# Kernel tuning notes

Hardware: AMD Instinct MI355X
Metric: run time of the kernel (lower is better)

Reference implementation:

```python
import jax, jax.numpy as jnp
import numpy as np

CROSSOVER_MAGNITUDE = 0.3
MUTATION_FACTOR = 0.3

B, A, H = 16, 512, 8  # batch, activation_size (== dim_emb), n_head


def setup_inputs() -> dict:
    key = jax.random.key(0)
    ks = jax.random.split(key, 11)
    d = A
    s = 0.02  # small init scale for weights
    return {
        "Q": jax.random.normal(ks[0], (B, A, A), jnp.float32),
        "K": jax.random.normal(ks[1], (B, A, A), jnp.float32),
        "V": jax.random.normal(ks[2], (B, A), jnp.float32),
        "WQ_w": jax.random.normal(ks[3], (d, d), jnp.float32) * s,
        "WQ_b": jax.random.normal(ks[4], (d,), jnp.float32) * s,
        "WK_w": jax.random.normal(ks[5], (d, d), jnp.float32) * s,
        "WK_b": jax.random.normal(ks[6], (d,), jnp.float32) * s,
        "WV_w": jax.random.normal(ks[7], (d, d), jnp.float32) * s,
        "WV_b": jax.random.normal(ks[8], (d,), jnp.float32) * s,
        "WO_w": jax.random.normal(ks[9], (d, d * H), jnp.float32) * s,
        "WO_b": jax.random.normal(ks[10], (d,), jnp.float32) * s,
    }


def _attention_core(Qp, Kp, Vp, WO_w, WO_b):
    # Qp, Kp: (B, A, A) projected; identical across heads in the original
    # (heads are copies stacked before shared Linear), so compute once
    # and broadcast. Vp: (B, A).
    rkey = jax.random.key(42)
    kp, km, kr1, kr2 = jax.random.split(rkey, 4)

    am0 = jnp.einsum('bji,bjk->bik', Qp, Kp) / jnp.sqrt(jnp.float32(8.0))
    am = jnp.broadcast_to(am0[:, None], (B, H, A, A))  # (B,H,A,A)

    def mutate(a):
        # elementwise multiply by U(1-mf, 1+mf) noise
        m = jax.random.uniform(km, a.shape, jnp.float32,
                               1.0 - MUTATION_FACTOR, 1.0 + MUTATION_FACTOR)
        return a * m

    def crossover(a):
        # swap the tail segments [c:] of two random rows per (batch, head)
        c = A - int(A * CROSSOVER_MAGNITUDE)
        r1 = jax.random.randint(kr1, (B, H), 0, A)
        r2 = jax.random.randint(kr2, (B, H), 0, A)
        bi = jnp.arange(B)[:, None]
        hi = jnp.arange(H)[None, :]
        tails = a[..., c:]                     # (B,H,A,A-c)
        t1 = tails[bi, hi, r1]                 # (B,H,A-c)
        t2 = tails[bi, hi, r2]
        tails = tails.at[bi, hi, r1].set(t2).at[bi, hi, r2].set(t1)
        return jnp.concatenate([a[..., :c], tails], axis=-1)

    p = jax.random.uniform(kp, ())
    am = jax.lax.cond(p <= 0.6, mutate, crossover, am)

    attn = jax.nn.softmax(am, axis=-1)               # (B,H,A,A)
    out = jnp.einsum('bhij,bj->bhi', attn, Vp)       # attn @ V[...,None] squeezed
    out = out.reshape(B, H * A)
    return out @ WO_w.T + WO_b                       # (B, A)


def reference(Q, K, V, WQ_w, WQ_b, WK_w, WK_b, WV_w, WV_b, WO_w, WO_b):
    Qp = Q @ WQ_w.T + WQ_b   # (B,A,A), same for every head
    Kp = K @ WK_w.T + WK_b
    Vp = V @ WV_w.T + WV_b   # (B,A)
    return _attention_core(Qp, Kp, Vp, WO_w, WO_b)
```

## Files before the change

### kernel.cpp

```cpp
#include <hip/hip_runtime.h>
#include <stdint.h>
#include <string.h>

#define B_ 16
#define A_ 512
#define H_ 8
#define C_CROSS 359
#define LDSTRIDE 40

typedef short short8 __attribute__((ext_vector_type(8)));
typedef float floatx4 __attribute__((ext_vector_type(4)));

__host__ __device__ __forceinline__ uint32_t rotl32(uint32_t x, int r) {
#ifdef __HIP_DEVICE_COMPILE__
  return __builtin_amdgcn_alignbit(x, x, 32 - r);
#else
  return (x << r) | (x >> (32 - r));
#endif
}

__host__ __device__ __forceinline__ void tf2x32(uint32_t k0, uint32_t k1,
                                                uint32_t x0, uint32_t x1,
                                                uint32_t& o0, uint32_t& o1) {
  uint32_t ks2 = k0 ^ k1 ^ 0x1BD11BDAu;
  x0 += k0; x1 += k1;
#define TFR(r) { x0 += x1; x1 = rotl32(x1, r); x1 ^= x0; }
  TFR(13) TFR(15) TFR(26) TFR(6)   x0 += k1;  x1 += ks2 + 1u;
  TFR(17) TFR(29) TFR(16) TFR(24)  x0 += ks2; x1 += k0 + 2u;
  TFR(13) TFR(15) TFR(26) TFR(6)   x0 += k0;  x1 += k1 + 3u;
  TFR(17) TFR(29) TFR(16) TFR(24)  x0 += k1;  x1 += ks2 + 4u;
  TFR(13) TFR(15) TFR(26) TFR(6)   x0 += ks2; x1 += k0 + 5u;
#undef TFR
  o0 = x0; o1 = x1;
}

__host__ __device__ __forceinline__ float bits2u01(uint32_t bits) {
  uint32_t v = (bits >> 9) | 0x3f800000u;
  float f;
#ifdef __HIP_DEVICE_COMPILE__
  f = __uint_as_float(v);
#else
  memcpy(&f, &v, 4);
#endif
  return f - 1.0f;
}

__device__ __forceinline__ float mutval(uint32_t km0, uint32_t km1, uint32_t L) {
  uint32_t a, b;
  tf2x32(km0, km1, 0u, L, a, b);
  float u = bits2u01(a ^ b);
  return fmaxf(0.7f, u * (1.3f - 0.7f) + 0.7f);
}

__device__ __forceinline__ uint32_t f2bf(float x) {
  uint32_t u = __float_as_uint(x);
  return (u + 0x7fffu + ((u >> 16) & 1u)) >> 16;
}
__device__ __forceinline__ float bf2f(uint32_t h) {
  return __uint_as_float(h << 16);
}

__device__ __forceinline__ void split8(const float* p, short8& h, short8& l) {
  float4 v0 = *(const float4*)p;
  float4 v1 = *(const float4*)(p + 4);
  float xs[8] = {v0.x, v0.y, v0.z, v0.w, v1.x, v1.y, v1.z, v1.w};
#pragma unroll
  for (int j = 0; j < 8; ++j) {
    uint32_t hb = f2bf(xs[j]);
    h[j] = (short)hb;
    l[j] = (short)f2bf(xs[j] - bf2f(hb));
  }
}

__global__ __launch_bounds__(256, 2) void lin_mfma2(
    const float* __restrict__ Xq, const float* __restrict__ Wq,
    const float* __restrict__ bq, ushort* __restrict__ QptH, ushort* __restrict__ QptL,
    const float* __restrict__ Xk, const float* __restrict__ Wk,
    const float* __restrict__ bk, ushort* __restrict__ KptH, ushort* __restrict__ KptL) {
  int bid = blockIdx.x;
  int z = bid >> 8;
  int rem = bid & 255;
  int ti = rem >> 2, tn = rem & 3;
  const float* X = z ? Xk : Xq;
  const float* W = z ? Wk : Wq;
  const float* bias = z ? bk : bq;
  ushort* OH = z ? KptH : QptH;
  ushort* OL = z ? KptL : QptL;

  __shared__ __align__(16) char smem[40960];
  ushort (*Ah)[LDSTRIDE] = (ushort(*)[LDSTRIDE])(smem);
  ushort (*Al)[LDSTRIDE] = (ushort(*)[LDSTRIDE])(smem + 10240);
  ushort (*Bh)[LDSTRIDE] = (ushort(*)[LDSTRIDE])(smem + 20480);
  ushort (*Bl)[LDSTRIDE] = (ushort(*)[LDSTRIDE])(smem + 30720);
  uint32_t (*cs)[132] = (uint32_t(*)[132])(smem);

  int tid = threadIdx.x;
  int w = tid >> 6, lane = tid & 63, quad = lane >> 4, l16 = lane & 15;
  int wm = (w >> 1) * 64, wn = (w & 1) * 64;
  int m0 = ti * 128;
  int n0 = tn * 128;

  float bv[4];
#pragma unroll
  for (int nt = 0; nt < 4; ++nt) bv[nt] = bias[n0 + wn + nt * 16 + l16];

  floatx4 acc[4][4] = {};

  for (int k0 = 0; k0 < 512; k0 += 32) {
    short8 ha[2], la[2], hb[2], lb[2];
#pragma unroll
    for (int g = 0; g < 2; ++g) {
      int gid = g * 256 + tid;
      int m = gid >> 2, kg = gid & 3;
      split8(X + (size_t)(m0 + m) * 512 + k0 + kg * 8, ha[g], la[g]);
      split8(W + (size_t)(n0 + m) * 512 + k0 + kg * 8, hb[g], lb[g]);
    }
    __syncthreads();
#pragma unroll
    for (int g = 0; g < 2; ++g) {
      int gid = g * 256 + tid;
      int m = gid >> 2, kg = gid & 3;
      *(short8*)&Ah[m][kg * 8] = ha[g];
      *(short8*)&Al[m][kg * 8] = la[g];
      *(short8*)&Bh[m][kg * 8] = hb[g];
      *(short8*)&Bl[m][kg * 8] = lb[g];
    }
    __syncthreads();
    short8 fAh[4], fAl[4], fBh[4], fBl[4];
#pragma unroll
    for (int t4 = 0; t4 < 4; ++t4) {
      int ma = wm + t4 * 16 + l16;
      int nb = wn + t4 * 16 + l16;
      fAh[t4] = *(const short8*)&Ah[ma][quad * 8];
      fAl[t4] = *(const short8*)&Al[ma][quad * 8];
      fBh[t4] = *(const short8*)&Bh[nb][quad * 8];
      fBl[t4] = *(const short8*)&Bl[nb][quad * 8];
    }
#pragma unroll
    for (int mt = 0; mt < 4; ++mt)
#pragma unroll
      for (int nt = 0; nt < 4; ++nt) {
        acc[mt][nt] = __builtin_amdgcn_mfma_f32_16x16x32_bf16(fAh[mt], fBh[nt], acc[mt][nt], 0, 0, 0);
        acc[mt][nt] = __builtin_amdgcn_mfma_f32_16x16x32_bf16(fAh[mt], fBl[nt], acc[mt][nt], 0, 0, 0);
        acc[mt][nt] = __builtin_amdgcn_mfma_f32_16x16x32_bf16(fAl[mt], fBh[nt], acc[mt][nt], 0, 0, 0);
      }
  }

  __syncthreads();
  int bb = m0 >> 9, i0 = m0 & 511;
  for (int p = 0; p < 2; ++p) {
    if ((w & 1) == p) {
#pragma unroll
      for (int mt = 0; mt < 4; ++mt)
#pragma unroll
        for (int nt = 0; nt < 4; ++nt)
#pragma unroll
          for (int rr = 0; rr < 4; ++rr) {
            float val = acc[mt][nt][rr] + bv[nt];
            uint32_t hb2 = f2bf(val);
            uint32_t lb2 = f2bf(val - bf2f(hb2));
            cs[nt * 16 + l16][wm + mt * 16 + quad * 4 + rr] = (hb2 << 16) | lb2;
          }
    }
    __syncthreads();
    {
      int col_l = tid >> 2, iseg = (tid & 3) * 32;
      int d = n0 + p * 64 + col_l;
      size_t obase = ((size_t)(bb * 512 + d)) * 512 + i0 + iseg;
      ushort* oh = OH + obase;
      ushort* ol = OL + obase;
#pragma unroll
      for (int sgi = 0; sgi < 4; ++sgi) {
        short8 hv, lv;
#pragma unroll
        for (int j = 0; j < 8; ++j) {
          uint32_t v = cs[col_l][iseg + sgi * 8 + j];
          hv[j] = (short)(v >> 16);
          lv[j] = (short)(v & 0xffffu);
        }
        *(short8*)(oh + sgi * 8) = hv;
        *(short8*)(ol + sgi * 8) = lv;
      }
    }
    __syncthreads();
  }
}

__global__ __launch_bounds__(256) void am_mfma2(
    const ushort* __restrict__ QH, const ushort* __restrict__ QL,
    const ushort* __restrict__ KH, const ushort* __restrict__ KL,
    float* __restrict__ am0) {
  int bid = blockIdx.x;
  int xcd = bid & 7, slot = bid >> 3;
  int bz = xcd + 8 * (slot >> 4);
  int tt = slot & 15, ti = tt >> 2, tk = tt & 3;
  int bm0 = ti * 128, bn0 = tk * 128;
  size_t base = (size_t)bz * 262144;
  const ushort* AHp = QH + base + (size_t)bm0 * 512;
  const ushort* ALp = QL + base + (size_t)bm0 * 512;
  const ushort* BHp = KH + base + (size_t)bn0 * 512;
  const ushort* BLp = KL + base + (size_t)bn0 * 512;

  __shared__ __align__(16) char smem[40960];
  ushort (*Ah)[LDSTRIDE] = (ushort(*)[LDSTRIDE])(smem);
  ushort (*Al)[LDSTRIDE] = (ushort(*)[LDSTRIDE])(smem + 10240);
  ushort (*Bh)[LDSTRIDE] = (ushort(*)[LDSTRIDE])(smem + 20480);
  ushort (*Bl)[LDSTRIDE] = (ushort(*)[LDSTRIDE])(smem + 30720);

  int tid = threadIdx.x;
  int w = tid >> 6, lane = tid & 63, quad = lane >> 4, l16 = lane & 15;
  int wm = (w >> 1) * 64, wn = (w & 1) * 64;

  floatx4 acc[4][4] = {};

  for (int k0 = 0; k0 < 512; k0 += 32) {
    short8 ha[2], la[2], hb[2], lb[2];
#pragma unroll
    for (int g = 0; g < 2; ++g) {
      int gid = g * 256 + tid;
      int m = gid >> 2, kg = gid & 3;
      size_t off = (size_t)m * 512 + k0 + kg * 8;
      ha[g] = *(const short8*)(AHp + off);
      la[g] = *(const short8*)(ALp + off);
      hb[g] = *(const short8*)(BHp + off);
      lb[g] = *(const short8*)(BLp + off);
    }
    __syncthreads();
#pragma unroll
    for (int g = 0; g < 2; ++g) {
      int gid = g * 256 + tid;
      int m = gid >> 2, kg = gid & 3;
      *(short8*)&Ah[m][kg * 8] = ha[g];
      *(short8*)&Al[m][kg * 8] = la[g];
      *(short8*)&Bh[m][kg * 8] = hb[g];
      *(short8*)&Bl[m][kg * 8] = lb[g];
    }
    __syncthreads();
    short8 fAh[4], fAl[4], fBh[4], fBl[4];
#pragma unroll
    for (int t4 = 0; t4 < 4; ++t4) {
      int ma = wm + t4 * 16 + l16;
      int nb = wn + t4 * 16 + l16;
      fAh[t4] = *(const short8*)&Ah[ma][quad * 8];
      fAl[t4] = *(const short8*)&Al[ma][quad * 8];
      fBh[t4] = *(const short8*)&Bh[nb][quad * 8];
      fBl[t4] = *(const short8*)&Bl[nb][quad * 8];
    }
#pragma unroll
    for (int mt = 0; mt < 4; ++mt)
#pragma unroll
      for (int nt = 0; nt < 4; ++nt) {
        acc[mt][nt] = __builtin_amdgcn_mfma_f32_16x16x32_bf16(fAh[mt], fBh[nt], acc[mt][nt], 0, 0, 0);
        acc[mt][nt] = __builtin_amdgcn_mfma_f32_16x16x32_bf16(fAh[mt], fBl[nt], acc[mt][nt], 0, 0, 0);
        acc[mt][nt] = __builtin_amdgcn_mfma_f32_16x16x32_bf16(fAl[mt], fBh[nt], acc[mt][nt], 0, 0, 0);
      }
  }
  const float scale = 0.35355339059327373f;
#pragma unroll
  for (int mt = 0; mt < 4; ++mt)
#pragma unroll
    for (int nt = 0; nt < 4; ++nt)
#pragma unroll
      for (int rr = 0; rr < 4; ++rr) {
        int row = bm0 + wm + mt * 16 + quad * 4 + rr;
        int col = bn0 + wn + nt * 16 + l16;
        am0[((size_t)(bz * 512 + row)) * 512 + col] = acc[mt][nt][rr] * scale;
      }
}

__global__ __launch_bounds__(256) void small_gemm(
    const float* __restrict__ X, const float* __restrict__ W,
    const float* __restrict__ bias, float* __restrict__ out, int K) {
  __shared__ float xs[16 * 260];
  __shared__ float ws[16 * 260];
  int tid = threadIdx.x;
  int j0 = blockIdx.x * 16;
  int k0 = blockIdx.y * 256;
#pragma unroll
  for (int it = 0; it < 4; ++it) {
    int idx = it * 256 + tid;
    int rr = idx >> 6, kk4 = idx & 63;
    float4 xv = *(const float4*)(X + (size_t)rr * K + k0 + kk4 * 4);
    float4 wv = *(const float4*)(W + (size_t)(j0 + rr) * K + k0 + kk4 * 4);
    *(float4*)&xs[rr * 260 + kk4 * 4] = xv;
    *(float4*)&ws[rr * 260 + kk4 * 4] = wv;
  }
  __syncthreads();
  int b = tid & 15, j = tid >> 4;
  const float* xr = &xs[b * 260];
  const float* wr = &ws[j * 260];
  float acc = 0.f;
#pragma unroll
  for (int kk = 0; kk < 256; kk += 4) {
    float4 a = *(const float4*)(xr + kk);
    float4 w4 = *(const float4*)(wr + kk);
    acc += a.x * w4.x + a.y * w4.y + a.z * w4.z + a.w * w4.w;
  }
  if (blockIdx.y == 0) acc += bias[j0 + j];
  atomicAdd(&out[b * 512 + j0 + j], acc);
}

__global__ __launch_bounds__(256) void soft_mut(
    const float* __restrict__ am0, const float* __restrict__ Vp,
    float* __restrict__ oa, uint32_t km0, uint32_t km1) {
  int tid = threadIdx.x;
  int w = tid >> 6, lane = tid & 63;
  int rrow = blockIdx.x * 4 + w;
  int b = rrow >> 12, h = (rrow >> 9) & 7, i = rrow & 511;
  const float* ar = am0 + ((size_t)((b << 9) + i)) * A_;
  const float* vr = Vp + (b << 9);
  uint32_t Lb = ((uint32_t)(((b * 8 + h) << 9) + i)) << 9;
  float x[8], vv[8];
#pragma unroll
  for (int j = 0; j < 8; ++j) {
    int k = lane + 64 * j;
    float a = ar[k];
    vv[j] = vr[k];
    x[j] = a * mutval(km0, km1, Lb + (uint32_t)k);
  }
  float s = 0.f, wsum = 0.f;
#pragma unroll
  for (int j = 0; j < 8; ++j) {
    float e = __expf(x[j]);
    s += e;
    wsum += e * vv[j];
  }
#pragma unroll
  for (int o = 32; o; o >>= 1) { s += __shfl_xor(s, o); wsum += __shfl_xor(wsum, o); }
  if (lane == 0) oa[(((size_t)(b * 8 + h)) << 9) + i] = wsum / s;
}

struct CrossCfg { int r1[B_ * H_]; int r2[B_ * H_]; };

__global__ __launch_bounds__(256) void soft_cross(
    const float* __restrict__ am0, const float* __restrict__ Vp,
    float* __restrict__ oa, CrossCfg cfg) {
  int tid = threadIdx.x;
  int w = tid >> 6, lane = tid & 63;
  int rrow = blockIdx.x * 4 + w;
  int b = rrow >> 12, h = (rrow >> 9) & 7, i = rrow & 511;
  int rr1 = cfg.r1[b * 8 + h], rr2 = cfg.r2[b * 8 + h];
  int src = (i == rr2) ? rr1 : ((i == rr1) ? rr2 : i);
  const float* ar = am0 + ((size_t)((b << 9) + i)) * A_;
  const float* ar2 = am0 + ((size_t)((b << 9) + src)) * A_;
  const float* vr = Vp + (b << 9);
  float x[8], vv[8];
#pragma unroll
  for (int j = 0; j < 8; ++j) {
    int k = lane + 64 * j;
    vv[j] = vr[k];
    x[j] = (k >= C_CROSS) ? ar2[k] : ar[k];
  }
  float s = 0.f, wsum = 0.f;
#pragma unroll
  for (int j = 0; j < 8; ++j) {
    float e = __expf(x[j]);
    s += e;
    wsum += e * vv[j];
  }
#pragma unroll
  for (int o = 32; o; o >>= 1) { s += __shfl_xor(s, o); wsum += __shfl_xor(wsum, o); }
  if (lane == 0) oa[(((size_t)(b * 8 + h)) << 9) + i] = wsum / s;
}

extern "C" void kernel_launch(void* const* d_in, const int* in_sizes, int n_in,
                              void* d_out, int out_size, void* d_ws, size_t ws_size,
                              hipStream_t stream) {
  (void)in_sizes; (void)n_in; (void)out_size; (void)ws_size;
  const float* Q    = (const float*)d_in[0];
  const float* K    = (const float*)d_in[1];
  const float* V    = (const float*)d_in[2];
  const float* WQ_w = (const float*)d_in[3];
  const float* WQ_b = (const float*)d_in[4];
  const float* WK_w = (const float*)d_in[5];
  const float* WK_b = (const float*)d_in[6];
  const float* WV_w = (const float*)d_in[7];
  const float* WV_b = (const float*)d_in[8];
  const float* WO_w = (const float*)d_in[9];
  const float* WO_b = (const float*)d_in[10];
  float* out = (float*)d_out;

  char* ws = (char*)d_ws;
  ushort* QptH = (ushort*)(ws);
  ushort* QptL = (ushort*)(ws + (size_t)8388608);
  ushort* KptH = (ushort*)(ws + (size_t)16777216);
  ushort* KptL = (ushort*)(ws + (size_t)25165824);
  float*  am0  = (float*) (ws + (size_t)33554432);
  float*  Vp   = (float*) (ws + (size_t)50331648);
  float*  oa   = (float*) (ws + (size_t)50331648 + 65536);

  uint32_t kp0, kp1, km0, km1, kr10, kr11, kr20, kr21, a, bbits;
  tf2x32(0u, 42u, 0u, 0u, kp0, kp1);
  tf2x32(0u, 42u, 0u, 1u, km0, km1);
  tf2x32(0u, 42u, 0u, 2u, kr10, kr11);
  tf2x32(0u, 42u, 0u, 3u, kr20, kr21);
  tf2x32(kp0, kp1, 0u, 0u, a, bbits);
  float p = bits2u01(a ^ bbits);
  if (p < 0.f) p = 0.f;
  bool mutate = (p <= 0.6f);

  hipMemsetAsync(Vp, 0, 16 * 512 * sizeof(float), stream);
  hipMemsetAsync(out, 0, 16 * 512 * sizeof(float), stream);

  lin_mfma2<<<512, 256, 0, stream>>>(Q, WQ_w, WQ_b, QptH, QptL,
                                     K, WK_w, WK_b, KptH, KptL);
  small_gemm<<<dim3(32, 2), 256, 0, stream>>>(V, WV_w, WV_b, Vp, 512);
  am_mfma2<<<256, 256, 0, stream>>>(QptH, QptL, KptH, KptL, am0);
  if (mutate) {
    soft_mut<<<16384, 256, 0, stream>>>(am0, Vp, oa, km0, km1);
  } else {
    CrossCfg cfg;
    uint32_t c0, c1;
    tf2x32(kr10, kr11, 0u, 1u, c0, c1);
    for (int t = 0; t < B_ * H_; ++t) {
      tf2x32(c0, c1, 0u, (uint32_t)t, a, bbits);
      cfg.r1[t] = (int)((a ^ bbits) & 511u);
    }
    tf2x32(kr20, kr21, 0u, 1u, c0, c1);
    for (int t = 0; t < B_ * H_; ++t) {
      tf2x32(c0, c1, 0u, (uint32_t)t, a, bbits);
      cfg.r2[t] = (int)((a ^ bbits) & 511u);
    }
    soft_cross<<<16384, 256, 0, stream>>>(am0, Vp, oa, cfg);
  }
  small_gemm<<<dim3(32, 16), 256, 0, stream>>>(oa, WO_w, WO_b, out, 4096);
}
```

Before: 250.7 us.

## Prefetch next K-tile into registers in GEMM kernels and simplify bf16 splitting

Both MFMA GEMM kernels now load the next K-slice from global memory into registers right after the LDS write barrier, so those loads overlap the MFMA work of the current slice. The fp32-to-bf16 hi/lo split switches from round-to-nearest to truncation, which needs fewer integer operations. am_mfma2 gets a min-blocks-per-CU launch bound of 2. The softmax kernels fuse the RNG and exp into a single loop with a folded FMA. Prefetching raises register pressure. Truncating the hi part slightly changes the hi/lo precision split.

```diff
diff --git a/kernel.cpp b/kernel.cpp
--- a/kernel.cpp
+++ b/kernel.cpp
@@ -45,30 +45,21 @@
   return f - 1.0f;
 }
 
-__device__ __forceinline__ float mutval(uint32_t km0, uint32_t km1, uint32_t L) {
-  uint32_t a, b;
-  tf2x32(km0, km1, 0u, L, a, b);
-  float u = bits2u01(a ^ b);
-  return fmaxf(0.7f, u * (1.3f - 0.7f) + 0.7f);
-}
-
-__device__ __forceinline__ uint32_t f2bf(float x) {
+__device__ __forceinline__ void tsplit(float x, short& h, short& l) {
   uint32_t u = __float_as_uint(x);
-  return (u + 0x7fffu + ((u >> 16) & 1u)) >> 16;
-}
-__device__ __forceinline__ float bf2f(uint32_t h) {
-  return __uint_as_float(h << 16);
-}
-
-__device__ __forceinline__ void split8(const float* p, short8& h, short8& l) {
-  float4 v0 = *(const float4*)p;
-  float4 v1 = *(const float4*)(p + 4);
+  float hf = __uint_as_float(u & 0xffff0000u);
+  h = (short)(u >> 16);
+  l = (short)(__float_as_uint(x - hf) >> 16);
+}
+
+__device__ __forceinline__ void tsplit8(const float4& v0, const float4& v1,
+                                        short8& h, short8& l) {
   float xs[8] = {v0.x, v0.y, v0.z, v0.w, v1.x, v1.y, v1.z, v1.w};
 #pragma unroll
   for (int j = 0; j < 8; ++j) {
-    uint32_t hb = f2bf(xs[j]);
-    h[j] = (short)hb;
-    l[j] = (short)f2bf(xs[j] - bf2f(hb));
+    short hh, ll;
+    tsplit(xs[j], hh, ll);
+    h[j] = hh; l[j] = ll;
   }
 }
 
@@ -104,28 +95,52 @@
 #pragma unroll
   for (int nt = 0; nt < 4; ++nt) bv[nt] = bias[n0 + wn + nt * 16 + l16];
 
+  const float* pX[2];
+  const float* pW[2];
+  int mW[2], kgW[2];
+#pragma unroll
+  for (int g = 0; g < 2; ++g) {
+    int gid = g * 256 + tid;
+    int m = gid >> 2, kg = gid & 3;
+    mW[g] = m; kgW[g] = kg;
+    pX[g] = X + (size_t)(m0 + m) * 512 + kg * 8;
+    pW[g] = W + (size_t)(n0 + m) * 512 + kg * 8;
+  }
+
+  float4 ra[2][2], rb[2][2];
+#pragma unroll
+  for (int g = 0; g < 2; ++g) {
+    ra[g][0] = *(const float4*)(pX[g]);
+    ra[g][1] = *(const float4*)(pX[g] + 4);
+    rb[g][0] = *(const float4*)(pW[g]);
+    rb[g][1] = *(const float4*)(pW[g] + 4);
+  }
+
   floatx4 acc[4][4] = {};
 
   for (int k0 = 0; k0 < 512; k0 += 32) {
-    short8 ha[2], la[2], hb[2], lb[2];
+    __syncthreads();
 #pragma unroll
     for (int g = 0; g < 2; ++g) {
-      int gid = g * 256 + tid;
-      int m = gid >> 2, kg = gid & 3;
-      split8(X + (size_t)(m0 + m) * 512 + k0 + kg * 8, ha[g], la[g]);
-      split8(W + (size_t)(n0 + m) * 512 + k0 + kg * 8, hb[g], lb[g]);
-    }
-    __syncthreads();
-#pragma unroll
-    for (int g = 0; g < 2; ++g) {
-      int gid = g * 256 + tid;
-      int m = gid >> 2, kg = gid & 3;
-      *(short8*)&Ah[m][kg * 8] = ha[g];
-      *(short8*)&Al[m][kg * 8] = la[g];
-      *(short8*)&Bh[m][kg * 8] = hb[g];
-      *(short8*)&Bl[m][kg * 8] = lb[g];
-    }
-    __syncthreads();
+      short8 h8, l8;
+      tsplit8(ra[g][0], ra[g][1], h8, l8);
+      *(short8*)&Ah[mW[g]][kgW[g] * 8] = h8;
+      *(short8*)&Al[mW[g]][kgW[g] * 8] = l8;
+      tsplit8(rb[g][0], rb[g][1], h8, l8);
+      *(short8*)&Bh[mW[g]][kgW[g] * 8] = h8;
+      *(short8*)&Bl[mW[g]][kgW[g] * 8] = l8;
+    }
+    __syncthreads();
+    if (k0 < 480) {
+      int kn = k0 + 32;
+#pragma unroll
+      for (int g = 0; g < 2; ++g) {
+        ra[g][0] = *(const float4*)(pX[g] + kn);
+        ra[g][1] = *(const float4*)(pX[g] + kn + 4);
+        rb[g][0] = *(const float4*)(pW[g] + kn);
+        rb[g][1] = *(const float4*)(pW[g] + kn + 4);
+      }
+    }
     short8 fAh[4], fAl[4], fBh[4], fBl[4];
 #pragma unroll
     for (int t4 = 0; t4 < 4; ++t4) {
@@ -157,9 +172,10 @@
 #pragma unroll
           for (int rr = 0; rr < 4; ++rr) {
             float val = acc[mt][nt][rr] + bv[nt];
-            uint32_t hb2 = f2bf(val);
-            uint32_t lb2 = f2bf(val - bf2f(hb2));
-            cs[nt * 16 + l16][wm + mt * 16 + quad * 4 + rr] = (hb2 << 16) | lb2;
+            uint32_t u = __float_as_uint(val);
+            uint32_t hi = u & 0xffff0000u;
+            uint32_t lo = __float_as_uint(val - __uint_as_float(hi)) >> 16;
+            cs[nt * 16 + l16][wm + mt * 16 + quad * 4 + rr] = hi | lo;
           }
     }
     __syncthreads();
@@ -186,7 +202,7 @@
   }
 }
 
-__global__ __launch_bounds__(256) void am_mfma2(
+__global__ __launch_bounds__(256, 2) void am_mfma2(
     const ushort* __restrict__ QH, const ushort* __restrict__ QL,
     const ushort* __restrict__ KH, const ushort* __restrict__ KL,
     float* __restrict__ am0) {
@@ -196,10 +212,6 @@
   int tt = slot & 15, ti = tt >> 2, tk = tt & 3;
   int bm0 = ti * 128, bn0 = tk * 128;
   size_t base = (size_t)bz * 262144;
-  const ushort* AHp = QH + base + (size_t)bm0 * 512;
-  const ushort* ALp = QL + base + (size_t)bm0 * 512;
-  const ushort* BHp = KH + base + (size_t)bn0 * 512;
-  const ushort* BLp = KL + base + (size_t)bn0 * 512;
 
   __shared__ __align__(16) char smem[40960];
   ushort (*Ah)[LDSTRIDE] = (ushort(*)[LDSTRIDE])(smem);
@@ -211,31 +223,50 @@
   int w = tid >> 6, lane = tid & 63, quad = lane >> 4, l16 = lane & 15;
   int wm = (w >> 1) * 64, wn = (w & 1) * 64;
 
+  const ushort *pAH[2], *pAL[2], *pBH[2], *pBL[2];
+  int mW[2], kgW[2];
+#pragma unroll
+  for (int g = 0; g < 2; ++g) {
+    int gid = g * 256 + tid;
+    int m = gid >> 2, kg = gid & 3;
+    mW[g] = m; kgW[g] = kg;
+    size_t offA = base + (size_t)(bm0 + m) * 512 + kg * 8;
+    size_t offB = base + (size_t)(bn0 + m) * 512 + kg * 8;
+    pAH[g] = QH + offA; pAL[g] = QL + offA;
+    pBH[g] = KH + offB; pBL[g] = KL + offB;
+  }
+
+  short8 rah[2], ral[2], rbh[2], rbl[2];
+#pragma unroll
+  for (int g = 0; g < 2; ++g) {
+    rah[g] = *(const short8*)(pAH[g]);
+    ral[g] = *(const short8*)(pAL[g]);
+    rbh[g] = *(const short8*)(pBH[g]);
+    rbl[g] = *(const short8*)(pBL[g]);
+  }
+
   floatx4 acc[4][4] = {};
 
   for (int k0 = 0; k0 < 512; k0 += 32) {
-    short8 ha[2], la[2], hb[2], lb[2];
+    __syncthreads();
 #pragma unroll
     for (int g = 0; g < 2; ++g) {
-      int gid = g * 256 + tid;
-      int m = gid >> 2, kg = gid & 3;
-      size_t off = (size_t)m * 512 + k0 + kg * 8;
-      ha[g] = *(const short8*)(AHp + off);
-      la[g] = *(const short8*)(ALp + off);
-      hb[g] = *(const short8*)(BHp + off);
-      lb[g] = *(const short8*)(BLp + off);
-    }
-    __syncthreads();
-#pragma unroll
-    for (int g = 0; g < 2; ++g) {
-      int gid = g * 256 + tid;
-      int m = gid >> 2, kg = gid & 3;
-      *(short8*)&Ah[m][kg * 8] = ha[g];
-      *(short8*)&Al[m][kg * 8] = la[g];
-      *(short8*)&Bh[m][kg * 8] = hb[g];
-      *(short8*)&Bl[m][kg * 8] = lb[g];
-    }
-    __syncthreads();
+      *(short8*)&Ah[mW[g]][kgW[g] * 8] = rah[g];
+      *(short8*)&Al[mW[g]][kgW[g] * 8] = ral[g];
+      *(short8*)&Bh[mW[g]][kgW[g] * 8] = rbh[g];
+      *(short8*)&Bl[mW[g]][kgW[g] * 8] = rbl[g];
+    }
+    __syncthreads();
+    if (k0 < 480) {
+      int kn = k0 + 32;
+#pragma unroll
+      for (int g = 0; g < 2; ++g) {
+        rah[g] = *(const short8*)(pAH[g] + kn);
+        ral[g] = *(const short8*)(pAL[g] + kn);
+        rbh[g] = *(const short8*)(pBH[g] + kn);
+        rbl[g] = *(const short8*)(pBL[g] + kn);
+      }
+    }
     short8 fAh[4], fAl[4], fBh[4], fBl[4];
 #pragma unroll
     for (int t4 = 0; t4 < 4; ++t4) {
@@ -307,23 +338,22 @@
   int w = tid >> 6, lane = tid & 63;
   int rrow = blockIdx.x * 4 + w;
   int b = rrow >> 12, h = (rrow >> 9) & 7, i = rrow & 511;
-  const float* ar = am0 + ((size_t)((b << 9) + i)) * A_;
-  const float* vr = Vp + (b << 9);
-  uint32_t Lb = ((uint32_t)(((b * 8 + h) << 9) + i)) << 9;
-  float x[8], vv[8];
+  const float* ar = am0 + ((size_t)((b << 9) + i)) * A_ + lane;
+  const float* vr = Vp + (b << 9) + lane;
+  uint32_t Lb = ((((uint32_t)(((b * 8 + h) << 9) + i)) << 9)) + (uint32_t)lane;
+  float s = 0.f, wsum = 0.f;
 #pragma unroll
   for (int j = 0; j < 8; ++j) {
-    int k = lane + 64 * j;
-    float a = ar[k];
-    vv[j] = vr[k];
-    x[j] = a * mutval(km0, km1, Lb + (uint32_t)k);
-  }
-  float s = 0.f, wsum = 0.f;
-#pragma unroll
-  for (int j = 0; j < 8; ++j) {
-    float e = __expf(x[j]);
+    float a = ar[64 * j];
+    float vv = vr[64 * j];
+    uint32_t o0, o1;
+    tf2x32(km0, km1, 0u, Lb + 64u * (uint32_t)j, o0, o1);
+    uint32_t bits = o0 ^ o1;
+    float f = __uint_as_float((bits >> 9) | 0x3f800000u);
+    float m = fmaxf(0.7f, __builtin_fmaf(f, 0.6f, 0.1f));
+    float e = __expf(a * m);
     s += e;
-    wsum += e * vv[j];
+    wsum += e * vv;
   }
 #pragma unroll
   for (int o = 32; o; o >>= 1) { s += __shfl_xor(s, o); wsum += __shfl_xor(wsum, o); }
@@ -344,19 +374,14 @@
   const float* ar = am0 + ((size_t)((b << 9) + i)) * A_;
   const float* ar2 = am0 + ((size_t)((b << 9) + src)) * A_;
   const float* vr = Vp + (b << 9);
-  float x[8], vv[8];
+  float s = 0.f, wsum = 0.f;
 #pragma unroll
   for (int j = 0; j < 8; ++j) {
     int k = lane + 64 * j;
-    vv[j] = vr[k];
-    x[j] = (k >= C_CROSS) ? ar2[k] : ar[k];
-  }
-  float s = 0.f, wsum = 0.f;
-#pragma unroll
-  for (int j = 0; j < 8; ++j) {
-    float e = __expf(x[j]);
+    float x = (k >= C_CROSS) ? ar2[k] : ar[k];
+    float e = __expf(x);
     s += e;
-    wsum += e * vv[j];
+    wsum += e * vr[k];
   }
 #pragma unroll
   for (int o = 32; o; o >>= 1) { s += __shfl_xor(s, o); wsum += __shfl_xor(wsum, o); }
```

After: 223.4 us. -10.9%, faster.
